# Performance work log

Hardware: AMD Instinct MI355X
Metric: run time of the kernel (lower is better)

Reference implementation:

```python
import jax, jax.numpy as jnp
import numpy as np

D_MODEL = 1024
N_HEADS = 16
HEAD_DIM = D_MODEL // N_HEADS


def setup_inputs() -> dict:
    key = jax.random.key(0)
    k_x, k_qkv, k_proj = jax.random.split(key, 3)
    x = jax.random.normal(k_x, (2, 2048, D_MODEL), dtype=jnp.float32)
    # flax nnx.Linear kernels: shape (in_features, out_features), lecun_normal-ish scale
    w_qkv = jax.random.normal(k_qkv, (D_MODEL, 3 * D_MODEL), dtype=jnp.float32) / np.sqrt(D_MODEL)
    w_proj = jax.random.normal(k_proj, (D_MODEL, D_MODEL), dtype=jnp.float32) / np.sqrt(D_MODEL)
    return {"x": x, "w_qkv": w_qkv, "w_proj": w_proj}


def reference(x, w_qkv, w_proj):
    bsz, seq_len, d_model = x.shape
    qkv = x @ w_qkv  # (B, T, 3*D)
    q, k, v = jnp.split(qkv, 3, axis=-1)
    q = q.reshape(bsz, seq_len, N_HEADS, HEAD_DIM)
    k = k.reshape(bsz, seq_len, N_HEADS, HEAD_DIM)
    v = v.reshape(bsz, seq_len, N_HEADS, HEAD_DIM)
    scale = jnp.sqrt(jnp.asarray(HEAD_DIM, dtype=x.dtype))
    attn_logits = jnp.einsum('bthd,bshd->bhts', q / scale, k)  # (B, H, T, T)
    attn_weights = jax.nn.softmax(attn_logits, axis=-1)
    attn_out = jnp.einsum('bhts,bshd->bthd', attn_weights, v)
    attn_out = attn_out.reshape(bsz, seq_len, d_model)
    return attn_out @ w_proj
```

## Files before the change

kernel.cpp:

```cpp
#include <hip/hip_runtime.h>
#include <hip/hip_bf16.h>
#include <cmath>

#define D_MODEL 1024
#define NH 16
#define HD 64
#define BSZ 2
#define SEQ 2048
#define MTOT (BSZ * SEQ)

typedef _Float16 f16x8 __attribute__((ext_vector_type(8)));
typedef __fp16   fp16x2 __attribute__((ext_vector_type(2)));
typedef float    f32x4  __attribute__((ext_vector_type(4)));
typedef float    f32x16 __attribute__((ext_vector_type(16)));
typedef unsigned int uivec2 __attribute__((ext_vector_type(2)));

#define QSCALE 0.18033688011112042f

__device__ __forceinline__ ushort f2h(float x) {
    union { _Float16 h; ushort u; } cv;
    cv.h = (_Float16)x;
    return cv.u;
}
__device__ __forceinline__ uint pkh(float a, float b) {
    union { fp16x2 h; uint u; } cv;
    cv.h = __builtin_amdgcn_cvt_pkrtz(a, b);
    return cv.u;
}
__device__ __forceinline__ float fexp2(float x) {
    float r; asm("v_exp_f32 %0, %1" : "=v"(r) : "v"(x)); return r;
}
__device__ __forceinline__ float fmax3(float a, float b, float c) {
    return fmaxf(fmaxf(a, b), c);
}
__device__ __forceinline__ void gload_lds16(const ushort* g, ushort* l) {
    __builtin_amdgcn_global_load_lds(
        (const __attribute__((address_space(1))) void*)g,
        (__attribute__((address_space(3))) void*)l, 16, 0, 0);
}

__global__ __launch_bounds__(256)
void cast8(const float* __restrict__ in, ushort* __restrict__ out, int n)
{
    const int i = (blockIdx.x * 256 + threadIdx.x) * 8;
    if (i >= n) return;
    float4 a = *(const float4*)(in + i);
    float4 b = *(const float4*)(in + i + 4);
    alignas(16) ushort h8[8];
    h8[0] = f2h(a.x); h8[1] = f2h(a.y); h8[2] = f2h(a.z); h8[3] = f2h(a.w);
    h8[4] = f2h(b.x); h8[5] = f2h(b.y); h8[6] = f2h(b.z); h8[7] = f2h(b.w);
    *(uint4*)(out + i) = *(const uint4*)h8;
}

__global__ __launch_bounds__(256)
void transpose_cast2(const float* __restrict__ A, const float* __restrict__ B,
                     ushort* __restrict__ At, ushort* __restrict__ Bt)
{
    __shared__ float tile[32][33];
    const int z = blockIdx.z;
    const float* in = (z < 3) ? A : B;
    ushort* out     = (z < 3) ? At : Bt;
    const int C     = (z < 3) ? 3 * D_MODEL : D_MODEL;
    const int cb    = (z < 3) ? z * 32 + blockIdx.x : blockIdx.x;
    const int R = D_MODEL;
    const int t  = threadIdx.x;
    const int r0 = blockIdx.y * 32, c0 = cb * 32;
    const int tr = t >> 5, tc = t & 31;
#pragma unroll
    for (int s = 0; s < 4; ++s)
        tile[tr + 8 * s][tc] = in[(size_t)(r0 + tr + 8 * s) * C + c0 + tc];
    __syncthreads();
#pragma unroll
    for (int s = 0; s < 4; ++s)
        out[(size_t)(c0 + tr + 8 * s) * R + r0 + tc] = f2h(tile[tc][tr + 8 * s]);
}

template <int MODE>
__global__ __launch_bounds__(256)
void gemm_mfma(const ushort* __restrict__ A, const ushort* __restrict__ Bt,
               float* __restrict__ outp,
               ushort* __restrict__ Qw, ushort* __restrict__ Kw,
               ushort* __restrict__ Vw, int N)
{
    __shared__ ushort As[3][128 * 32];
    __shared__ ushort Bs[3][128 * 32];

    const int t  = threadIdx.x;
    const int w  = t >> 6;
    const int l  = t & 63;
    const int lr = l & 15;
    const int lg = l >> 4;
    const int wr = w >> 1, wc = w & 1;
    const int m0 = blockIdx.y * 128, n0 = blockIdx.x * 128;

    const ushort* Ab = A  + (size_t)m0 * 1024;
    const ushort* Bb = Bt + (size_t)n0 * 1024;

    f32x4 acc[4][4];
#pragma unroll
    for (int i = 0; i < 4; ++i)
#pragma unroll
        for (int j = 0; j < 4; ++j) acc[i][j] = (f32x4){0.f, 0.f, 0.f, 0.f};

    auto stage = [&](int buf, int kt) {
        const int k0 = kt * 32;
#pragma unroll
        for (int s = 0; s < 2; ++s) {
            const int c    = s * 64 + l;
            const int row  = w * 32 + (c >> 2);
            const int unit = c & 3;
            gload_lds16(Ab + (size_t)row * 1024 + k0 + unit * 8,
                        &As[buf][(w * 128 + s * 64) * 8]);
            gload_lds16(Bb + (size_t)row * 1024 + k0 + unit * 8,
                        &Bs[buf][(w * 128 + s * 64) * 8]);
        }
    };

    auto body = [&](int kt, int cb, int vm) {
        if (kt + 2 < 32) stage((cb + 2) % 3, kt + 2);
        if (vm == 8)      asm volatile("s_waitcnt vmcnt(8)" ::: "memory");
        else if (vm == 4) asm volatile("s_waitcnt vmcnt(4)" ::: "memory");
        else              asm volatile("s_waitcnt vmcnt(0)" ::: "memory");
        __builtin_amdgcn_s_barrier();

        f16x8 af[4], bf[4];
#pragma unroll
        for (int m = 0; m < 4; ++m)
            af[m] = *(const f16x8*)&As[cb][(wr * 64 + m * 16 + lr) * 32 + lg * 8];
#pragma unroll
        for (int n = 0; n < 4; ++n)
            bf[n] = *(const f16x8*)&Bs[cb][(wc * 64 + n * 16 + lr) * 32 + lg * 8];
        __builtin_amdgcn_s_setprio(1);
#pragma unroll
        for (int m = 0; m < 4; ++m)
#pragma unroll
            for (int n = 0; n < 4; ++n)
                acc[m][n] = __builtin_amdgcn_mfma_f32_16x16x32_f16(
                    af[m], bf[n], acc[m][n], 0, 0, 0);
        __builtin_amdgcn_s_setprio(0);
        __builtin_amdgcn_s_barrier();
    };

    stage(0, 0);
    stage(1, 1);
#pragma unroll 1
    for (int i = 0; i < 10; ++i) {
        body(i * 3 + 0, 0, 8);
        body(i * 3 + 1, 1, 8);
        body(i * 3 + 2, 2, 8);
    }
    body(30, 0, 4);
    body(31, 1, 0);

    if (MODE == 1) {
#pragma unroll
        for (int mf = 0; mf < 4; ++mf) {
            const int row = m0 + wr * 64 + mf * 16 + lg * 4;
#pragma unroll
            for (int nf = 0; nf < 4; ++nf) {
                const int col = n0 + wc * 64 + nf * 16 + lr;
#pragma unroll
                for (int i = 0; i < 4; ++i)
                    outp[(size_t)(row + i) * N + col] = acc[mf][nf][i];
            }
        }
    } else {
#pragma unroll
        for (int mf = 0; mf < 4; ++mf) {
            const int row = m0 + wr * 64 + mf * 16 + lg * 4;
            const int b   = row >> 11;
            const int tt0 = row & (SEQ - 1);
#pragma unroll
            for (int nf = 0; nf < 4; ++nf) {
                const int col   = n0 + wc * 64 + nf * 16 + lr;
                const int which = col >> 10;
                const int h     = (col >> 6) & 15;
                const int d     = col & 63;
                if (which == 2) {
                    ushort* p = Vw + (((size_t)(b * NH + h) * HD + d) * SEQ) + tt0;
                    alignas(8) ushort e4[4];
#pragma unroll
                    for (int i = 0; i < 4; ++i) e4[i] = f2h(acc[mf][nf][i]);
                    *(uint2*)p = *(const uint2*)e4;
                } else {
                    ushort* dst = (which == 0) ? Qw : Kw;
                    const float sc = (which == 0) ? QSCALE : 1.0f;
#pragma unroll
                    for (int i = 0; i < 4; ++i)
                        dst[((size_t)(b * NH + h) * SEQ + tt0 + i) * HD + d] =
                            f2h(acc[mf][nf][i] * sc);
                }
            }
        }
    }
}

__global__ __launch_bounds__(512, 4)
void attn_mfma7(const ushort* __restrict__ Qw, const ushort* __restrict__ Kw,
                const ushort* __restrict__ Vtg, ushort* __restrict__ AO)
{
    __shared__ ushort KsAll[2][2][64 * 64];
    __shared__ ushort VtAll[2][2][64 * 64];

    const int t    = threadIdx.x;
    const int w    = t >> 6;
    const int l    = t & 63;
    const int q    = l & 31;
    const int hi   = l >> 5;
    const int half = w >> 2;
    const int ww   = w & 3;

    const int bh = blockIdx.y;
    const int q0 = blockIdx.x * 128 + ww * 32;
    const int kbase = half * (SEQ / 2);
    const int NT = (SEQ / 2) / 64;

    const ushort* Qp = Qw  + (size_t)bh * SEQ * HD;
    const ushort* Kp = Kw  + (size_t)bh * SEQ * HD;
    const ushort* Vp = Vtg + (size_t)bh * HD * SEQ;

    ushort (*Ks)[64 * 64] = KsAll[half];
    ushort (*Vt)[64 * 64] = VtAll[half];

    f16x8 qf[4];
#pragma unroll
    for (int kc = 0; kc < 4; ++kc)
        qf[kc] = *(const f16x8*)(Qp + (size_t)(q0 + q) * HD + kc * 16 + hi * 8);

    f32x16 oacc[2];
#pragma unroll
    for (int db = 0; db < 2; ++db)
#pragma unroll
        for (int r = 0; r < 16; ++r) oacc[db][r] = 0.f;
    float m_run = -3.0e38f, l_run = 0.f;

    auto stageK = [&](int buf, int k0) {
#pragma unroll
        for (int s = 0; s < 2; ++s) {
            const int c    = ww * 64 + l + 256 * s;
            const int row  = c >> 3;
            const int unit = (c & 7) ^ (row & 7);
            gload_lds16(Kp + (size_t)(k0 + row) * HD + unit * 8,
                        &Ks[buf][(ww * 64 + 256 * s) * 8]);
        }
    };
    auto stageV = [&](int buf, int k0) {
#pragma unroll
        for (int s = 0; s < 2; ++s) {
            const int c    = ww * 64 + l + 256 * s;
            const int row  = c >> 3;
            const int unit = (c & 7) ^ (row & 7);
            gload_lds16(Vp + (size_t)row * SEQ + k0 + unit * 8,
                        &Vt[buf][(ww * 64 + 256 * s) * 8]);
        }
    };

    stageK(0, kbase);
    stageV(0, kbase);
    __syncthreads();

    int cur = 0;
    for (int kt = 0; kt < NT; ++kt) {
        if (kt + 1 < NT) {
            stageK(cur ^ 1, kbase + (kt + 1) * 64);
            stageV(cur ^ 1, kbase + (kt + 1) * 64);
        }

        f32x16 sacc[2];
        __builtin_amdgcn_s_setprio(1);
#pragma unroll
        for (int kb = 0; kb < 2; ++kb) {
            f32x16 a;
#pragma unroll
            for (int r = 0; r < 16; ++r) a[r] = 0.f;
            const int row = kb * 32 + q;
            const int swz = (row & 7) << 4;
#pragma unroll
            for (int kc = 0; kc < 4; ++kc) {
                f16x8 kf = *(const f16x8*)(
                    (const char*)Ks[cur] + row * 128 + ((kc * 32 + hi * 16) ^ swz));
                a = __builtin_amdgcn_mfma_f32_32x32x16_f16(kf, qf[kc], a, 0, 0, 0);
            }
            sacc[kb] = a;
        }
        __builtin_amdgcn_s_setprio(0);

        float p0 = fmax3(fmaxf(sacc[0][0], sacc[1][0]),
                         fmaxf(sacc[0][1], sacc[1][1]),
                         fmaxf(sacc[0][2], sacc[1][2]));
        float p1 = fmax3(fmaxf(sacc[0][3], sacc[1][3]),
                         fmaxf(sacc[0][4], sacc[1][4]),
                         fmaxf(sacc[0][5], sacc[1][5]));
        float p2 = fmax3(fmaxf(sacc[0][6], sacc[1][6]),
                         fmaxf(sacc[0][7], sacc[1][7]),
                         fmaxf(sacc[0][8], sacc[1][8]));
        float p3 = fmax3(fmaxf(sacc[0][9], sacc[1][9]),
                         fmaxf(sacc[0][10], sacc[1][10]),
                         fmaxf(sacc[0][11], sacc[1][11]));
        float p4 = fmax3(fmaxf(sacc[0][12], sacc[1][12]),
                         fmaxf(sacc[0][13], sacc[1][13]),
                         fmaxf(sacc[0][14], sacc[1][14]));
        float p5 = fmaxf(sacc[0][15], sacc[1][15]);
        float mx = fmaxf(fmax3(p0, p1, p2), fmax3(p3, p4, p5));
        mx = fmaxf(mx, __shfl_xor(mx, 32));

        if (__any(mx > m_run + 8.0f)) {
            const float m_new = fmaxf(m_run, mx);
            const float scale = fexp2(m_run - m_new);
            m_run = m_new;
            l_run *= scale;
#pragma unroll
            for (int db = 0; db < 2; ++db)
#pragma unroll
                for (int r = 0; r < 16; ++r) oacc[db][r] *= scale;
        }

#pragma unroll
        for (int kb = 0; kb < 2; ++kb)
#pragma unroll
            for (int r = 0; r < 16; ++r)
                sacc[kb][r] = fexp2(sacc[kb][r] - m_run);

        float ts[16];
#pragma unroll
        for (int r = 0; r < 16; ++r) ts[r] = sacc[0][r] + sacc[1][r];
#pragma unroll
        for (int s = 8; s > 0; s >>= 1)
#pragma unroll
            for (int r = 0; r < 8; ++r)
                if (r < s) ts[r] += ts[r + s];
        l_run += ts[0] + __shfl_xor(ts[0], 32);

        f16x8 pfrag[4];
#pragma unroll
        for (int kb = 0; kb < 2; ++kb)
#pragma unroll
            for (int lc = 0; lc < 2; ++lc) {
                const int rb = lc * 8;
                uint a = pkh(sacc[kb][rb + 0], sacc[kb][rb + 1]);
                uint b = pkh(sacc[kb][rb + 2], sacc[kb][rb + 3]);
                uint c = pkh(sacc[kb][rb + 4], sacc[kb][rb + 5]);
                uint d = pkh(sacc[kb][rb + 6], sacc[kb][rb + 7]);
                uivec2 r0 = __builtin_amdgcn_permlane32_swap(a, c, false, false);
                uivec2 r1 = __builtin_amdgcn_permlane32_swap(b, d, false, false);
                union { uint u[4]; f16x8 v; } f;
                f.u[0] = r0.x;
                f.u[1] = r1.x;
                f.u[2] = r0.y;
                f.u[3] = r1.y;
                pfrag[kb * 2 + lc] = f.v;
            }

        __builtin_amdgcn_s_setprio(1);
#pragma unroll
        for (int db = 0; db < 2; ++db) {
            const int row = db * 32 + q;
            const int swz = (row & 7) << 4;
#pragma unroll
            for (int kc = 0; kc < 4; ++kc) {
                f16x8 vf = *(const f16x8*)(
                    (const char*)Vt[cur] + row * 128 + ((kc * 32 + hi * 16) ^ swz));
                oacc[db] = __builtin_amdgcn_mfma_f32_32x32x16_f16(
                    vf, pfrag[kc], oacc[db], 0, 0, 0);
            }
        }
        __builtin_amdgcn_s_setprio(0);

        __syncthreads();
        cur ^= 1;
    }

    float* oex = (float*)KsAll;
    float* mex = (float*)VtAll;
    float* lex = mex + 256;

    if (half == 1) {
        mex[ww * 64 + l] = m_run;
        lex[ww * 64 + l] = l_run;
#pragma unroll
        for (int db = 0; db < 2; ++db)
#pragma unroll
            for (int r = 0; r < 16; ++r)
                oex[(((ww * 2 + db) * 16) + r) * 64 + l] = oacc[db][r];
    }
    __syncthreads();
    if (half == 0) {
        const float m2 = mex[ww * 64 + l];
        const float l2 = lex[ww * 64 + l];
        const float mf = fmaxf(m_run, m2);
        float w1 = fexp2(m_run - mf), w2 = fexp2(m2 - mf);
        const float inv = 1.f / (l_run * w1 + l2 * w2);
        w1 *= inv; w2 *= inv;

        const int b = bh >> 4, h = bh & 15;
        ushort* orow = AO + ((size_t)(b * SEQ) + q0 + q) * D_MODEL + h * HD;
#pragma unroll
        for (int db = 0; db < 2; ++db)
#pragma unroll
            for (int g = 0; g < 4; ++g) {
                const int d = db * 32 + g * 8 + hi * 4;
                alignas(8) ushort e4[4];
#pragma unroll
                for (int i = 0; i < 4; ++i) {
                    const float o2 = oex[(((ww * 2 + db) * 16) + g * 4 + i) * 64 + l];
                    e4[i] = f2h(oacc[db][g * 4 + i] * w1 + o2 * w2);
                }
                *(uint2*)(orow + d) = *(const uint2*)e4;
            }
    }
}

extern "C" void kernel_launch(void* const* d_in, const int* in_sizes, int n_in,
                              void* d_out, int out_size, void* d_ws, size_t ws_size,
                              hipStream_t stream)
{
    const float* x      = (const float*)d_in[0];
    const float* w_qkv  = (const float*)d_in[1];
    const float* w_proj = (const float*)d_in[2];
    float* out = (float*)d_out;

    ushort* Xh  = (ushort*)d_ws;
    ushort* WqT = Xh  + (size_t)MTOT * D_MODEL;
    ushort* WpT = WqT + (size_t)3 * D_MODEL * D_MODEL;
    ushort* Qw  = WpT + (size_t)D_MODEL * D_MODEL;
    ushort* Kw  = Qw  + (size_t)MTOT * D_MODEL;
    ushort* Vt  = Kw  + (size_t)MTOT * D_MODEL;
    ushort* AOh = Vt  + (size_t)MTOT * D_MODEL;

    dim3 blk(256);

    cast8<<<dim3(MTOT * D_MODEL / (8 * 256)), blk, 0, stream>>>(x, Xh, MTOT * D_MODEL);
    transpose_cast2<<<dim3(32, 32, 4), blk, 0, stream>>>(w_qkv, w_proj, WqT, WpT);

    gemm_mfma<0><<<dim3(3 * D_MODEL / 128, MTOT / 128), blk, 0, stream>>>(
        Xh, WqT, nullptr, Qw, Kw, Vt, 3 * D_MODEL);

    attn_mfma7<<<dim3(SEQ / 128, BSZ * NH), dim3(512), 0, stream>>>(Qw, Kw, Vt, AOh);

    gemm_mfma<1><<<dim3(D_MODEL / 128, MTOT / 128), blk, 0, stream>>>(
        AOh, WpT, out, nullptr, nullptr, nullptr, D_MODEL);
}
```

Baseline: 137.6 us.

## Fuse x fp32-to-fp16 cast into QKV GEMM and add XCD-aware block swizzle

Removes the separate cast kernel over x. The QKV GEMM now loads fp32 rows of x through registers, converts them to fp16 and writes them into shared memory one stage ahead, while B still uses direct global-to-LDS loads. Both GEMMs also remap block indices so that consecutive workgroups spread across the 8 XCDs and neighbouring tiles share an XCD's cache. This saves a full write and re-read of the fp16 activation and one launch, at the cost of twice the global bytes for A inside the GEMM plus extra register pressure and conversion work in the main loop.

After: 142.5 us. +3.6%, slower.

```diff
diff --git a/kernel.cpp b/kernel.cpp
--- a/kernel.cpp
+++ b/kernel.cpp
@@ -37,19 +37,6 @@
     __builtin_amdgcn_global_load_lds(
         (const __attribute__((address_space(1))) void*)g,
         (__attribute__((address_space(3))) void*)l, 16, 0, 0);
-}
-
-__global__ __launch_bounds__(256)
-void cast8(const float* __restrict__ in, ushort* __restrict__ out, int n)
-{
-    const int i = (blockIdx.x * 256 + threadIdx.x) * 8;
-    if (i >= n) return;
-    float4 a = *(const float4*)(in + i);
-    float4 b = *(const float4*)(in + i + 4);
-    alignas(16) ushort h8[8];
-    h8[0] = f2h(a.x); h8[1] = f2h(a.y); h8[2] = f2h(a.z); h8[3] = f2h(a.w);
-    h8[4] = f2h(b.x); h8[5] = f2h(b.y); h8[6] = f2h(b.z); h8[7] = f2h(b.w);
-    *(uint4*)(out + i) = *(const uint4*)h8;
 }
 
 __global__ __launch_bounds__(256)
@@ -75,12 +62,10 @@
         out[(size_t)(c0 + tr + 8 * s) * R + r0 + tc] = f2h(tile[tc][tr + 8 * s]);
 }
 
-template <int MODE>
 __global__ __launch_bounds__(256)
-void gemm_mfma(const ushort* __restrict__ A, const ushort* __restrict__ Bt,
-               float* __restrict__ outp,
-               ushort* __restrict__ Qw, ushort* __restrict__ Kw,
-               ushort* __restrict__ Vw, int N)
+void gemm_qkv(const float* __restrict__ A, const ushort* __restrict__ Bt,
+              ushort* __restrict__ Qw, ushort* __restrict__ Kw,
+              ushort* __restrict__ Vw)
 {
     __shared__ ushort As[3][128 * 32];
     __shared__ ushort Bs[3][128 * 32];
@@ -91,7 +76,142 @@
     const int lr = l & 15;
     const int lg = l >> 4;
     const int wr = w >> 1, wc = w & 1;
-    const int m0 = blockIdx.y * 128, n0 = blockIdx.x * 128;
+
+    const int gx   = gridDim.x;
+    const int nwg  = gx * gridDim.y;
+    const int lin  = blockIdx.y * gx + blockIdx.x;
+    const int lin2 = (lin & 7) * (nwg >> 3) + (lin >> 3);
+    const int m0   = (lin2 / gx) * 128;
+    const int n0   = (lin2 % gx) * 128;
+
+    const float*  Ab = A  + (size_t)m0 * 1024;
+    const ushort* Bb = Bt + (size_t)n0 * 1024;
+
+    f32x4 acc[4][4];
+#pragma unroll
+    for (int i = 0; i < 4; ++i)
+#pragma unroll
+        for (int j = 0; j < 4; ++j) acc[i][j] = (f32x4){0.f, 0.f, 0.f, 0.f};
+
+    const int arow = w * 32 + (l >> 3);
+    const int acol = (l & 7) * 4;
+    float4 ar[4];
+    auto loadA = [&](int kt) {
+#pragma unroll
+        for (int s = 0; s < 4; ++s)
+            ar[s] = *(const float4*)(Ab + (size_t)(arow + s * 8) * 1024
+                                        + kt * 32 + acol);
+    };
+    auto writeA = [&](int buf) {
+#pragma unroll
+        for (int s = 0; s < 4; ++s) {
+            alignas(8) ushort e4[4];
+            e4[0] = f2h(ar[s].x); e4[1] = f2h(ar[s].y);
+            e4[2] = f2h(ar[s].z); e4[3] = f2h(ar[s].w);
+            *(uint2*)&As[buf][(arow + s * 8) * 32 + acol] = *(const uint2*)e4;
+        }
+    };
+    auto stageB = [&](int buf, int kt) {
+#pragma unroll
+        for (int s = 0; s < 2; ++s) {
+            const int c    = s * 64 + l;
+            const int row  = w * 32 + (c >> 2);
+            const int unit = c & 3;
+            gload_lds16(Bb + (size_t)row * 1024 + kt * 32 + unit * 8,
+                        &Bs[buf][(w * 128 + s * 64) * 8]);
+        }
+    };
+
+    auto body = [&](int kt, int cb, int vm) {
+        if (vm == 2) asm volatile("s_waitcnt vmcnt(2)" ::: "memory");
+        else         asm volatile("s_waitcnt vmcnt(0)" ::: "memory");
+        asm volatile("s_waitcnt lgkmcnt(0)" ::: "memory");
+        __builtin_amdgcn_s_barrier();
+
+        if (kt + 1 < 32) writeA((cb + 1) % 3);
+        if (kt + 2 < 32) { loadA(kt + 2); stageB((cb + 2) % 3, kt + 2); }
+
+        f16x8 af[4], bf[4];
+#pragma unroll
+        for (int m = 0; m < 4; ++m)
+            af[m] = *(const f16x8*)&As[cb][(wr * 64 + m * 16 + lr) * 32 + lg * 8];
+#pragma unroll
+        for (int n = 0; n < 4; ++n)
+            bf[n] = *(const f16x8*)&Bs[cb][(wc * 64 + n * 16 + lr) * 32 + lg * 8];
+        __builtin_amdgcn_s_setprio(1);
+#pragma unroll
+        for (int m = 0; m < 4; ++m)
+#pragma unroll
+            for (int n = 0; n < 4; ++n)
+                acc[m][n] = __builtin_amdgcn_mfma_f32_16x16x32_f16(
+                    af[m], bf[n], acc[m][n], 0, 0, 0);
+        __builtin_amdgcn_s_setprio(0);
+        __builtin_amdgcn_s_barrier();
+    };
+
+    loadA(0); stageB(0, 0);
+    asm volatile("s_waitcnt vmcnt(2)" ::: "memory");
+    writeA(0);
+    loadA(1); stageB(1, 1);
+
+#pragma unroll 1
+    for (int i = 0; i < 10; ++i) {
+        body(i * 3 + 0, 0, 2);
+        body(i * 3 + 1, 1, 2);
+        body(i * 3 + 2, 2, 2);
+    }
+    body(30, 0, 2);
+    body(31, 1, 0);
+
+#pragma unroll
+    for (int mf = 0; mf < 4; ++mf) {
+        const int row = m0 + wr * 64 + mf * 16 + lg * 4;
+        const int b   = row >> 11;
+        const int tt0 = row & (SEQ - 1);
+#pragma unroll
+        for (int nf = 0; nf < 4; ++nf) {
+            const int col   = n0 + wc * 64 + nf * 16 + lr;
+            const int which = col >> 10;
+            const int h     = (col >> 6) & 15;
+            const int d     = col & 63;
+            if (which == 2) {
+                ushort* p = Vw + (((size_t)(b * NH + h) * HD + d) * SEQ) + tt0;
+                alignas(8) ushort e4[4];
+#pragma unroll
+                for (int i = 0; i < 4; ++i) e4[i] = f2h(acc[mf][nf][i]);
+                *(uint2*)p = *(const uint2*)e4;
+            } else {
+                ushort* dst = (which == 0) ? Qw : Kw;
+                const float sc = (which == 0) ? QSCALE : 1.0f;
+#pragma unroll
+                for (int i = 0; i < 4; ++i)
+                    dst[((size_t)(b * NH + h) * SEQ + tt0 + i) * HD + d] =
+                        f2h(acc[mf][nf][i] * sc);
+            }
+        }
+    }
+}
+
+__global__ __launch_bounds__(256)
+void gemm_proj(const ushort* __restrict__ A, const ushort* __restrict__ Bt,
+               float* __restrict__ outp)
+{
+    __shared__ ushort As[3][128 * 32];
+    __shared__ ushort Bs[3][128 * 32];
+
+    const int t  = threadIdx.x;
+    const int w  = t >> 6;
+    const int l  = t & 63;
+    const int lr = l & 15;
+    const int lg = l >> 4;
+    const int wr = w >> 1, wc = w & 1;
+
+    const int gx   = gridDim.x;
+    const int nwg  = gx * gridDim.y;
+    const int lin  = blockIdx.y * gx + blockIdx.x;
+    const int lin2 = (lin & 7) * (nwg >> 3) + (lin >> 3);
+    const int m0   = (lin2 / gx) * 128;
+    const int n0   = (lin2 % gx) * 128;
 
     const ushort* Ab = A  + (size_t)m0 * 1024;
     const ushort* Bb = Bt + (size_t)n0 * 1024;
@@ -152,45 +272,15 @@
     body(30, 0, 4);
     body(31, 1, 0);
 
-    if (MODE == 1) {
-#pragma unroll
-        for (int mf = 0; mf < 4; ++mf) {
-            const int row = m0 + wr * 64 + mf * 16 + lg * 4;
-#pragma unroll
-            for (int nf = 0; nf < 4; ++nf) {
-                const int col = n0 + wc * 64 + nf * 16 + lr;
-#pragma unroll
-                for (int i = 0; i < 4; ++i)
-                    outp[(size_t)(row + i) * N + col] = acc[mf][nf][i];
-            }
-        }
-    } else {
-#pragma unroll
-        for (int mf = 0; mf < 4; ++mf) {
-            const int row = m0 + wr * 64 + mf * 16 + lg * 4;
-            const int b   = row >> 11;
-            const int tt0 = row & (SEQ - 1);
-#pragma unroll
-            for (int nf = 0; nf < 4; ++nf) {
-                const int col   = n0 + wc * 64 + nf * 16 + lr;
-                const int which = col >> 10;
-                const int h     = (col >> 6) & 15;
-                const int d     = col & 63;
-                if (which == 2) {
-                    ushort* p = Vw + (((size_t)(b * NH + h) * HD + d) * SEQ) + tt0;
-                    alignas(8) ushort e4[4];
-#pragma unroll
-                    for (int i = 0; i < 4; ++i) e4[i] = f2h(acc[mf][nf][i]);
-                    *(uint2*)p = *(const uint2*)e4;
-                } else {
-                    ushort* dst = (which == 0) ? Qw : Kw;
-                    const float sc = (which == 0) ? QSCALE : 1.0f;
-#pragma unroll
-                    for (int i = 0; i < 4; ++i)
-                        dst[((size_t)(b * NH + h) * SEQ + tt0 + i) * HD + d] =
-                            f2h(acc[mf][nf][i] * sc);
-                }
-            }
+#pragma unroll
+    for (int mf = 0; mf < 4; ++mf) {
+        const int row = m0 + wr * 64 + mf * 16 + lg * 4;
+#pragma unroll
+        for (int nf = 0; nf < 4; ++nf) {
+            const int col = n0 + wc * 64 + nf * 16 + lr;
+#pragma unroll
+            for (int i = 0; i < 4; ++i)
+                outp[(size_t)(row + i) * 1024 + col] = acc[mf][nf][i];
         }
     }
 }
@@ -419,8 +509,7 @@
     const float* w_proj = (const float*)d_in[2];
     float* out = (float*)d_out;
 
-    ushort* Xh  = (ushort*)d_ws;
-    ushort* WqT = Xh  + (size_t)MTOT * D_MODEL;
+    ushort* WqT = (ushort*)d_ws;
     ushort* WpT = WqT + (size_t)3 * D_MODEL * D_MODEL;
     ushort* Qw  = WpT + (size_t)D_MODEL * D_MODEL;
     ushort* Kw  = Qw  + (size_t)MTOT * D_MODEL;
@@ -429,14 +518,12 @@
 
     dim3 blk(256);
 
-    cast8<<<dim3(MTOT * D_MODEL / (8 * 256)), blk, 0, stream>>>(x, Xh, MTOT * D_MODEL);
     transpose_cast2<<<dim3(32, 32, 4), blk, 0, stream>>>(w_qkv, w_proj, WqT, WpT);
 
-    gemm_mfma<0><<<dim3(3 * D_MODEL / 128, MTOT / 128), blk, 0, stream>>>(
-        Xh, WqT, nullptr, Qw, Kw, Vt, 3 * D_MODEL);
+    gemm_qkv<<<dim3(3 * D_MODEL / 128, MTOT / 128), blk, 0, stream>>>(
+        x, WqT, Qw, Kw, Vt);
 
     attn_mfma7<<<dim3(SEQ / 128, BSZ * NH), dim3(512), 0, stream>>>(Qw, Kw, Vt, AOh);
 
-    gemm_mfma<1><<<dim3(D_MODEL / 128, MTOT / 128), blk, 0, stream>>>(
-        AOh, WpT, out, nullptr, nullptr, nullptr, D_MODEL);
-}
+    gemm_proj<<<dim3(D_MODEL / 128, MTOT / 128), blk, 0, stream>>>(AOh, WpT, out);
+}
```
